# Performance work log

Measured on AMD Instinct MI355X. Metric: run time of the kernel, lower is better.

Reference implementation:

```python
import jax, jax.numpy as jnp
import numpy as np

EMBED_DIM = 32
HIDDEN_DIM = 64
N = 1024
LN_EPS = 1e-5


def setup_inputs() -> dict:
    key = jax.random.key(0)
    ks = jax.random.split(key, 8)
    d, h = EMBED_DIM, HIDDEN_DIM
    s1 = 1.0 / np.sqrt(2 * d)
    s2 = 1.0 / np.sqrt(h)
    return {
        "node_embeddings": jax.random.normal(ks[0], (N, d), dtype=jnp.float32),
        # Linear(2d -> h), stored as (2d, h) for x @ W
        "W1": jax.random.uniform(ks[1], (2 * d, h), jnp.float32, -s1, s1),
        "b1": jnp.zeros((h,), jnp.float32),
        "g1": jnp.ones((h,), jnp.float32),
        "be1": jnp.zeros((h,), jnp.float32),
        "W2": jax.random.uniform(ks[2], (h, h), jnp.float32, -s2, s2),
        "b2": jnp.zeros((h,), jnp.float32),
        "g2": jnp.ones((h,), jnp.float32),
        "be2": jnp.zeros((h,), jnp.float32),
        "W3": jax.random.uniform(ks[3], (h, 1), jnp.float32, -s2, s2),
        "b3": jnp.zeros((1,), jnp.float32),
    }


def _layernorm(x, gamma, beta):
    mu = jnp.mean(x, axis=-1, keepdims=True)
    var = jnp.mean(jnp.square(x - mu), axis=-1, keepdims=True)
    return (x - mu) * jax.lax.rsqrt(var + LN_EPS) * gamma + beta


def reference(node_embeddings, W1, b1, g1, be1, W2, b2, g2, be2, W3, b3):
    n, d = node_embeddings.shape
    # pair_emb = cat([src_emb, dst_emb], -1); first linear applied without
    # materializing the concat: split W1 into src/dst halves.
    W1s, W1d = W1[:d], W1[d:]
    hs = node_embeddings @ W1s          # (N, h)
    hd = node_embeddings @ W1d          # (N, h)
    h = hs[:, None, :] + hd[None, :, :] + b1   # (N, N, h)
    h = jax.nn.relu(_layernorm(h, g1, be1))
    h = jax.nn.relu(_layernorm(h @ W2 + b2, g2, be2))
    out = jax.nn.sigmoid((h @ W3 + b3)[..., 0])  # (N, N)
    return out
```

## Files before the change

kernel.cpp:

```cpp
#include <hip/hip_runtime.h>
#include <hip/hip_bf16.h>

#define NN 1024
#define ED 32
#define HD 64
#define LN_EPS 1e-5f

typedef short bf16x8 __attribute__((ext_vector_type(8)));
typedef float f32x4 __attribute__((ext_vector_type(4)));

#define OFF_HS   0
#define OFF_HDB  65536
#define OFF_SS   131072
#define OFF_SD   132096
#define OFF_G1   133120
#define OFF_BE1  133184
#define OFF_B2   133248
#define OFF_G2   133312
#define OFF_BE2  133376
#define OFF_W3   133440
#define OFF_B3   133504
#define OFF_SB2  133505
#define OFF_W2F  133508

__device__ __forceinline__ bool buf_is_f32(const void* g1) {
  return *(const unsigned int*)g1 == 0x3F800000u;
}
template <bool F32>
__device__ __forceinline__ float ld(const void* p, int i) {
  return F32 ? ((const float*)p)[i]
             : __bfloat162float(((const __hip_bfloat16*)p)[i]);
}
__device__ __forceinline__ unsigned short f2bf(float f) {
  unsigned int b = __builtin_bit_cast(unsigned int, f);
  b += 0x7FFFu + ((b >> 16) & 1u);
  return (unsigned short)(b >> 16);
}
__device__ __forceinline__ unsigned int pack2bf(float a, float b) {
  return (unsigned int)f2bf(a) | ((unsigned int)f2bf(b) << 16);
}
__device__ __forceinline__ unsigned int pk_bf(float a, float b) {
  __hip_bfloat162 p = __float22bfloat162_rn(make_float2(a, b));
  unsigned int u;
  __builtin_memcpy(&u, &p, 4);
  return u;
}
__device__ __forceinline__ f32x4 splat4(float v) { f32x4 r = {v, v, v, v}; return r; }

template <int CTRL>
__device__ __forceinline__ float dpp_add(float v) {
  int m = __builtin_amdgcn_update_dpp(0, __builtin_bit_cast(int, v), CTRL, 0xF, 0xF, true);
  return v + __builtin_bit_cast(float, m);
}
__device__ __forceinline__ float red16(float v) {
  v = dpp_add<0xB1>(v);
  v = dpp_add<0x4E>(v);
  v = dpp_add<0x124>(v);
  v = dpp_add<0x128>(v);
  return v;
}

template <bool F32>
__device__ void prep_body(const void* E, const void* W1, const void* b1,
                          const void* g1, const void* be1, const void* W2,
                          const void* b2, const void* g2, const void* be2,
                          const void* W3, const void* b3, float* ws) {
  const int i = blockIdx.x, t = threadIdx.x;
  if (i < NN) {
    __shared__ float e[ED];
    if (t < ED) e[t] = ld<F32>(E, i * ED + t);
    __syncthreads();
    int k = t & 63;
    bool dside = t >= 64;
    int wofs = dside ? ED * HD : 0;
    float acc = 0.f;
#pragma unroll
    for (int c = 0; c < ED; ++c)
      acc = fmaf(e[c], ld<F32>(W1, wofs + c * HD + k), acc);
    if (dside) acc += ld<F32>(b1, k);
    float s = acc;
#pragma unroll
    for (int m = 1; m <= 32; m <<= 1) s += __shfl_xor(s, m);
    if (dside) {
      ws[OFF_HDB + i * HD + k] = acc;
      if (k == 0) ws[OFF_SD + i] = s;
    } else {
      ws[OFF_HS + i * HD + k] = acc;
      if (k == 0) ws[OFF_SS + i] = s;
    }
  } else if (i < NN + 16) {
    if (t < 32) {
      int d = (i - NN) * 32 + t;
      int lv = d & 63, nt = (d >> 6) & 3, kc = d >> 8;
      int k0 = kc * 32 + ((lv >> 4) & 3) * 8;
      int n = nt * 16 + (lv & 15);
      unsigned int u4[4];
#pragma unroll
      for (int jj = 0; jj < 4; ++jj)
        u4[jj] = pack2bf(ld<F32>(W2, (k0 + 2 * jj) * HD + n),
                         ld<F32>(W2, (k0 + 2 * jj + 1) * HD + n));
      ((uint4*)(ws + OFF_W2F))[d] = make_uint4(u4[0], u4[1], u4[2], u4[3]);
    }
  } else {
    __shared__ float rs[64];
    if (t < 64) {
      ws[OFF_G1  + t] = ld<F32>(g1,  t);
      ws[OFF_BE1 + t] = ld<F32>(be1, t);
      ws[OFF_B2  + t] = ld<F32>(b2,  t);
      ws[OFF_G2  + t] = ld<F32>(g2,  t);
      ws[OFF_BE2 + t] = ld<F32>(be2, t);
      ws[OFF_W3  + t] = ld<F32>(W3,  t);
      float s = 0.f;
      for (int n = 0; n < HD; ++n) s += ld<F32>(W2, t * HD + n);
      rs[t] = s;
    }
    if (t == 64) {
      float s = 0.f;
      for (int n = 0; n < HD; ++n) s += ld<F32>(b2, n);
      ws[OFF_SB2] = s;
    }
    if (t == 65) ws[OFF_B3] = ld<F32>(b3, 0);
    __syncthreads();
    unsigned short* st = (unsigned short*)(ws + OFF_W2F) + 4096;
    for (int s = t; s < 1024; s += 128) {
      int j = s & 7, lv = (s >> 3) & 63, kc = s >> 9;
      st[s] = f2bf(rs[kc * 32 + ((lv >> 4) & 3) * 8 + j]);
    }
  }
}

__global__ __launch_bounds__(128) void prep_kern(
    const void* E, const void* W1, const void* b1, const void* g1,
    const void* be1, const void* W2, const void* b2, const void* g2,
    const void* be2, const void* W3, const void* b3, float* ws) {
  if (buf_is_f32(g1))
    prep_body<true >(E, W1, b1, g1, be1, W2, b2, g2, be2, W3, b3, ws);
  else
    prep_body<false>(E, W1, b1, g1, be1, W2, b2, g2, be2, W3, b3, ws);
}

__global__ __launch_bounds__(256, 4) void pair_kern(
    const float* __restrict__ ws, float* __restrict__ out) {
  __shared__ float sh[1024];
  __shared__ float sdt[1024];
  __shared__ __align__(16) unsigned int X[256 * 32];
  const int t = threadIdx.x;
  const int bi = blockIdx.y, bj = blockIdx.x;
  const int l = t & 63, w = t >> 6;
  const int q = l >> 4, ln = l & 15;
  const float inv = 1.f / 64.f;

  {
    int r = t >> 4, c4 = t & 15;
    ((f32x4*)sh )[r * 16 + (c4 ^ r)] = ((const f32x4*)(ws + OFF_HS  + (bi * 16 + r) * HD))[c4];
    ((f32x4*)sdt)[r * 16 + (c4 ^ r)] = ((const f32x4*)(ws + OFF_HDB + (bj * 16 + r) * HD))[c4];
  }
  const int il = t >> 4, jl = t & 15;
  const float ssum = ws[OFF_SS + bi * 16 + il];
  const float dsum = ws[OFF_SD + bj * 16 + jl];
  __syncthreads();

  {
    const f32x4* A4 = (const f32x4*)sh;
    const f32x4* B4 = (const f32x4*)sdt;
    f32x4 xv[16];
    f32x4 q4 = splat4(0.f);
#pragma unroll
    for (int c = 0; c < 16; ++c) {
      f32x4 x = A4[il * 16 + (c ^ il)] + B4[jl * 16 + (c ^ jl)];
      xv[c] = x;
      q4 = __builtin_elementwise_fma(x, x, q4);
    }
    float ssq = (q4[0] + q4[1]) + (q4[2] + q4[3]);
    float mu = (ssum + dsum) * inv;
    float r1 = rsqrtf(fmaf(-mu, mu, ssq * inv) + LN_EPS);
    f32x4 r1v = splat4(r1), nm = splat4(-mu * r1), zero = splat4(0.f);
    uint4* Xr4 = (uint4*)(X + t * 32);
#pragma unroll
    for (int b = 0; b < 8; ++b) {
      unsigned int uu[4];
#pragma unroll
      for (int h = 0; h < 2; ++h) {
        int c = 2 * b + h;
        f32x4 g, be;
#pragma unroll
        for (int e = 0; e < 4; ++e) {
          g[e]  = ws[OFF_G1  + c * 4 + e];
          be[e] = ws[OFF_BE1 + c * 4 + e];
        }
        f32x4 u = __builtin_elementwise_fma(xv[c], r1v, nm);
        f32x4 v = __builtin_elementwise_fma(u, g, be);
        v = __builtin_elementwise_max(v, zero);
        uu[2 * h]     = pk_bf(v[0], v[1]);
        uu[2 * h + 1] = pk_bf(v[2], v[3]);
      }
      Xr4[b ^ (t & 7)] = make_uint4(uu[0], uu[1], uu[2], uu[3]);
    }
  }

  bf16x8 bf[2][4], bsum[2];
  const uint4* WF4 = (const uint4*)(ws + OFF_W2F);
#pragma unroll
  for (int kc = 0; kc < 2; ++kc) {
#pragma unroll
    for (int nt = 0; nt < 4; ++nt)
      bf[kc][nt] = __builtin_bit_cast(bf16x8, WF4[(kc * 4 + nt) * 64 + l]);
    bsum[kc] = __builtin_bit_cast(bf16x8, WF4[512 + kc * 64 + l]);
  }
  f32x4 acc[4][5];
  const uint4* XL = (const uint4*)X;
#pragma unroll
  for (int mt = 0; mt < 4; ++mt) {
    int m = w * 64 + mt * 16 + ln;
    bf16x8 a0 = __builtin_bit_cast(bf16x8, XL[m * 8 + (q ^ (m & 7))]);
    bf16x8 a1 = __builtin_bit_cast(bf16x8, XL[m * 8 + ((q + 4) ^ (m & 7))]);
#pragma unroll
    for (int nt = 0; nt < 5; ++nt) {
      bf16x8 b0  = (nt < 4) ? bf[0][nt] : bsum[0];
      bf16x8 b1f = (nt < 4) ? bf[1][nt] : bsum[1];
      f32x4 z4 = splat4(0.f);
      z4 = __builtin_amdgcn_mfma_f32_16x16x32_bf16(a0, b0, z4, 0, 0, 0);
      acc[mt][nt] = __builtin_amdgcn_mfma_f32_16x16x32_bf16(a1, b1f, z4, 0, 0, 0);
    }
  }

  float b2v[4], g2v[4], be2v[4], w3v[4];
#pragma unroll
  for (int nt = 0; nt < 4; ++nt) {
    int cix = nt * 16 + ln;
    b2v[nt]  = ws[OFF_B2  + cix];
    g2v[nt]  = ws[OFF_G2  + cix];
    be2v[nt] = ws[OFF_BE2 + cix];
    w3v[nt]  = ws[OFF_W3  + cix];
  }
  const float b3s = ws[OFF_B3];
  const float Sb2 = ws[OFF_SB2];

#pragma unroll
  for (int mt = 0; mt < 4; ++mt) {
    f32x4 y[4], qq = splat4(0.f);
#pragma unroll
    for (int nt = 0; nt < 4; ++nt) {
      y[nt] = acc[mt][nt] + splat4(b2v[nt]);
      qq = __builtin_elementwise_fma(y[nt], y[nt], qq);
    }
#pragma unroll
    for (int e = 0; e < 4; ++e) qq[e] = red16(qq[e]);
    f32x4 s4 = acc[mt][4] + splat4(Sb2);
    f32x4 mu = s4 * inv;
    f32x4 var = qq * inv - mu * mu;
    f32x4 r2;
#pragma unroll
    for (int e = 0; e < 4; ++e) r2[e] = rsqrtf(var[e] + LN_EPS);
    f32x4 z4 = splat4(0.f);
#pragma unroll
    for (int nt = 0; nt < 4; ++nt) {
      f32x4 u = (y[nt] - mu) * r2;
      f32x4 v = __builtin_elementwise_fma(u, splat4(g2v[nt]), splat4(be2v[nt]));
      v = __builtin_elementwise_max(v, splat4(0.f));
      z4 = __builtin_elementwise_fma(v, splat4(w3v[nt]), z4);
    }
#pragma unroll
    for (int e = 0; e < 4; ++e) z4[e] = red16(z4[e]);
    float z01 = (ln & 1) ? z4[1] : z4[0];
    float z23 = (ln & 1) ? z4[3] : z4[2];
    float zs = ((ln & 2) ? z23 : z01) + b3s;
    float o = 1.f / (1.f + __expf(-zs));
    if (ln < 4)
      out[(bi * 16 + w * 4 + mt) * NN + bj * 16 + q * 4 + ln] = o;
  }
}

extern "C" void kernel_launch(void* const* d_in, const int* in_sizes, int n_in,
                              void* d_out, int out_size, void* d_ws, size_t ws_size,
                              hipStream_t stream) {
  float* ws = (float*)d_ws;
  hipLaunchKernelGGL(prep_kern, dim3(NN + 17), dim3(128), 0, stream,
                     d_in[0], d_in[1], d_in[2], d_in[3], d_in[4], d_in[5],
                     d_in[6], d_in[7], d_in[8], d_in[9], d_in[10], ws);
  hipLaunchKernelGGL(pair_kern, dim3(64, 64), dim3(256), 0, stream,
                     ws, (float*)d_out);
}
```

Measured before the change: 118.9 us.

## Drop LDS staging of hs/hd, fold b2 into MFMA init, remap blocks for XCD locality

Each thread now reads its hs and hd rows straight from global memory instead of staging them in shared memory. That removes two LDS arrays and a __syncthreads, and launch bounds are raised to 5 blocks per CU. The b2 bias and its sum are loaded into the MFMA accumulator init, so the separate bias add disappears. Blocks move to a 1D grid with a remapping that spreads tiles across the 8 XCDs, and every lane writes one sigmoid output instead of only 4 of 16 lanes per row. The risk is redundant uncoalesced global reads per thread and higher register pressure under the tighter occupancy target.

```diff
diff --git a/kernel.cpp b/kernel.cpp
--- a/kernel.cpp
+++ b/kernel.cpp
@@ -139,35 +139,29 @@
     prep_body<false>(E, W1, b1, g1, be1, W2, b2, g2, be2, W3, b3, ws);
 }
 
-__global__ __launch_bounds__(256, 4) void pair_kern(
+__global__ __launch_bounds__(256, 5) void pair_kern(
     const float* __restrict__ ws, float* __restrict__ out) {
-  __shared__ float sh[1024];
-  __shared__ float sdt[1024];
   __shared__ __align__(16) unsigned int X[256 * 32];
   const int t = threadIdx.x;
-  const int bi = blockIdx.y, bj = blockIdx.x;
+  const int bid = blockIdx.x;
+  const int lid = (bid & 7) * 512 + (bid >> 3);
+  const int bi = lid >> 6, bj = lid & 63;
   const int l = t & 63, w = t >> 6;
   const int q = l >> 4, ln = l & 15;
+  const int il = t >> 4, jl = t & 15;
   const float inv = 1.f / 64.f;
 
-  {
-    int r = t >> 4, c4 = t & 15;
-    ((f32x4*)sh )[r * 16 + (c4 ^ r)] = ((const f32x4*)(ws + OFF_HS  + (bi * 16 + r) * HD))[c4];
-    ((f32x4*)sdt)[r * 16 + (c4 ^ r)] = ((const f32x4*)(ws + OFF_HDB + (bj * 16 + r) * HD))[c4];
-  }
-  const int il = t >> 4, jl = t & 15;
   const float ssum = ws[OFF_SS + bi * 16 + il];
   const float dsum = ws[OFF_SD + bj * 16 + jl];
-  __syncthreads();
 
   {
-    const f32x4* A4 = (const f32x4*)sh;
-    const f32x4* B4 = (const f32x4*)sdt;
+    const f32x4* A4 = (const f32x4*)(ws + OFF_HS  + (bi * 16 + il) * HD);
+    const f32x4* B4 = (const f32x4*)(ws + OFF_HDB + (bj * 16 + jl) * HD);
     f32x4 xv[16];
     f32x4 q4 = splat4(0.f);
 #pragma unroll
     for (int c = 0; c < 16; ++c) {
-      f32x4 x = A4[il * 16 + (c ^ il)] + B4[jl * 16 + (c ^ jl)];
+      f32x4 x = A4[c] + B4[c];
       xv[c] = x;
       q4 = __builtin_elementwise_fma(x, x, q4);
     }
@@ -198,6 +192,11 @@
     }
   }
 
+  float b2v[4];
+#pragma unroll
+  for (int nt = 0; nt < 4; ++nt) b2v[nt] = ws[OFF_B2 + nt * 16 + ln];
+  const float Sb2 = ws[OFF_SB2];
+
   bf16x8 bf[2][4], bsum[2];
   const uint4* WF4 = (const uint4*)(ws + OFF_W2F);
 #pragma unroll
@@ -218,57 +217,55 @@
     for (int nt = 0; nt < 5; ++nt) {
       bf16x8 b0  = (nt < 4) ? bf[0][nt] : bsum[0];
       bf16x8 b1f = (nt < 4) ? bf[1][nt] : bsum[1];
-      f32x4 z4 = splat4(0.f);
+      f32x4 z4 = splat4(nt < 4 ? b2v[nt] : Sb2);
       z4 = __builtin_amdgcn_mfma_f32_16x16x32_bf16(a0, b0, z4, 0, 0, 0);
       acc[mt][nt] = __builtin_amdgcn_mfma_f32_16x16x32_bf16(a1, b1f, z4, 0, 0, 0);
     }
   }
 
-  float b2v[4], g2v[4], be2v[4], w3v[4];
+  float g2v[4], be2v[4], w3v[4];
 #pragma unroll
   for (int nt = 0; nt < 4; ++nt) {
     int cix = nt * 16 + ln;
-    b2v[nt]  = ws[OFF_B2  + cix];
     g2v[nt]  = ws[OFF_G2  + cix];
     be2v[nt] = ws[OFF_BE2 + cix];
     w3v[nt]  = ws[OFF_W3  + cix];
   }
   const float b3s = ws[OFF_B3];
-  const float Sb2 = ws[OFF_SB2];
+  const int mkeep = (l >> 2) & 3;
+  float zkeep = 0.f;
 
 #pragma unroll
   for (int mt = 0; mt < 4; ++mt) {
-    f32x4 y[4], qq = splat4(0.f);
+    f32x4 qq = splat4(0.f);
+#pragma unroll
+    for (int nt = 0; nt < 4; ++nt)
+      qq = __builtin_elementwise_fma(acc[mt][nt], acc[mt][nt], qq);
+#pragma unroll
+    for (int e = 0; e < 4; ++e) qq[e] = red16(qq[e]);
+    f32x4 mu = acc[mt][4] * splat4(inv);
+    f32x4 var = __builtin_elementwise_fma(qq, splat4(inv), -(mu * mu));
+    f32x4 r2, nm2;
+#pragma unroll
+    for (int e = 0; e < 4; ++e) r2[e] = rsqrtf(var[e] + LN_EPS);
+    nm2 = -(mu * r2);
+    f32x4 z4 = splat4(0.f);
 #pragma unroll
     for (int nt = 0; nt < 4; ++nt) {
-      y[nt] = acc[mt][nt] + splat4(b2v[nt]);
-      qq = __builtin_elementwise_fma(y[nt], y[nt], qq);
-    }
-#pragma unroll
-    for (int e = 0; e < 4; ++e) qq[e] = red16(qq[e]);
-    f32x4 s4 = acc[mt][4] + splat4(Sb2);
-    f32x4 mu = s4 * inv;
-    f32x4 var = qq * inv - mu * mu;
-    f32x4 r2;
-#pragma unroll
-    for (int e = 0; e < 4; ++e) r2[e] = rsqrtf(var[e] + LN_EPS);
-    f32x4 z4 = splat4(0.f);
-#pragma unroll
-    for (int nt = 0; nt < 4; ++nt) {
-      f32x4 u = (y[nt] - mu) * r2;
+      f32x4 u = __builtin_elementwise_fma(acc[mt][nt], r2, nm2);
       f32x4 v = __builtin_elementwise_fma(u, splat4(g2v[nt]), splat4(be2v[nt]));
       v = __builtin_elementwise_max(v, splat4(0.f));
       z4 = __builtin_elementwise_fma(v, splat4(w3v[nt]), z4);
     }
 #pragma unroll
     for (int e = 0; e < 4; ++e) z4[e] = red16(z4[e]);
-    float z01 = (ln & 1) ? z4[1] : z4[0];
-    float z23 = (ln & 1) ? z4[3] : z4[2];
-    float zs = ((ln & 2) ? z23 : z01) + b3s;
-    float o = 1.f / (1.f + __expf(-zs));
-    if (ln < 4)
-      out[(bi * 16 + w * 4 + mt) * NN + bj * 16 + q * 4 + ln] = o;
-  }
+    float z01 = (l & 1) ? z4[1] : z4[0];
+    float z23 = (l & 1) ? z4[3] : z4[2];
+    float zl  = (l & 2) ? z23 : z01;
+    zkeep = (mkeep == mt) ? zl : zkeep;
+  }
+  float o = 1.f / (1.f + __expf(-(zkeep + b3s)));
+  out[(bi * 16 + w * 4 + mkeep) * NN + bj * 16 + q * 4 + (l & 3)] = o;
 }
 
 extern "C" void kernel_launch(void* const* d_in, const int* in_sizes, int n_in,
@@ -278,6 +275,6 @@
   hipLaunchKernelGGL(prep_kern, dim3(NN + 17), dim3(128), 0, stream,
                      d_in[0], d_in[1], d_in[2], d_in[3], d_in[4], d_in[5],
                      d_in[6], d_in[7], d_in[8], d_in[9], d_in[10], ws);
-  hipLaunchKernelGGL(pair_kern, dim3(64, 64), dim3(256), 0, stream,
+  hipLaunchKernelGGL(pair_kern, dim3(4096), dim3(256), 0, stream,
                      ws, (float*)d_out);
 }
```

Result: slower. 175.7 us (+47.8%).
